# Performance work log

Hardware: AMD Instinct MI355X
Metric: run time of the kernel (lower is better)

## Reference

```python
import jax, jax.numpy as jnp
import numpy as np

EPS = 1e-15
N_NODES = 20000
N_EDGES = 640000
FEAT = 128
N_RBF = 20
CUTOFF = 5.0


def setup_inputs() -> dict:
    key = jax.random.key(0)
    ks = jax.random.split(key, 10)
    s_j = jax.random.normal(ks[0], (N_NODES, FEAT), jnp.float32)
    v_j = jax.random.normal(ks[1], (N_NODES, FEAT, 3), jnp.float32)
    r_ij = jax.random.normal(ks[2], (N_EDGES, 3), jnp.float32)
    nbrs = jax.random.randint(ks[3], (N_EDGES, 2), 0, N_NODES, jnp.int64)
    # InvariantDense: Dense(F->F, swish) then Dense(F->3F)
    W1 = jax.random.normal(ks[4], (FEAT, FEAT), jnp.float32) / np.sqrt(FEAT)
    b1 = jnp.zeros((FEAT,), jnp.float32)
    W2 = jax.random.normal(ks[5], (FEAT, 3 * FEAT), jnp.float32) / np.sqrt(FEAT)
    b2 = jnp.zeros((3 * FEAT,), jnp.float32)
    # DistanceEmbed dense: Dense(n_rbf -> 3F)
    Wd = jax.random.normal(ks[6], (N_RBF, 3 * FEAT), jnp.float32) / np.sqrt(N_RBF)
    bd = jnp.zeros((3 * FEAT,), jnp.float32)
    return {"s_j": s_j, "v_j": v_j, "r_ij": r_ij, "nbrs": nbrs,
            "W1": W1, "b1": b1, "W2": W2, "b2": b2, "Wd": Wd, "bd": bd}


def reference(s_j, v_j, r_ij, nbrs, W1, b1, W2, b2, Wd, bd):
    N, F = s_j.shape
    # preprocess_r
    dist = jnp.sqrt(jnp.sum(r_ij ** 2 + EPS, axis=-1))          # [E]
    unit = r_ij / dist[:, None]                                  # [E,3]
    # InvariantDense on nodes (dense before gather, as in torch code)
    phi_node = jax.nn.silu(s_j @ W1 + b1) @ W2 + b2              # [N,3F]
    phi = phi_node[nbrs[:, 1]]                                   # [E,3F]
    # PaiNN radial basis: sin(n*pi*d/cutoff)/d, n=1..n_rbf
    k = jnp.arange(1, N_RBF + 1, dtype=dist.dtype) * (np.pi / CUTOFF)  # [n_rbf]
    rbf = jnp.sin(dist[:, None] * k[None, :]) / dist[:, None]    # [E,n_rbf]
    # cosine cutoff envelope
    env = 0.5 * (jnp.cos(np.pi * dist / CUTOFF) + 1.0)
    env = jnp.where(dist < CUTOFF, env, 0.0)                     # [E]
    w_s = (rbf @ Wd + bd) * env[:, None]                         # [E,3F]
    inv = (phi * w_s).reshape(-1, 3, F)                          # [E,3,F]
    split0 = inv[:, 0, :][:, :, None]                            # [E,F,1]
    split1 = inv[:, 1, :]                                        # [E,F]
    split2 = inv[:, 2, :][:, :, None]                            # [E,F,1]
    delta_v_ij = split2 * unit[:, None, :] + split0 * v_j[nbrs[:, 1]]  # [E,F,3]
    idx = nbrs[:, 0]
    delta_s_i = jax.ops.segment_sum(split1, idx, num_segments=N)      # [N,F]
    delta_v_i = jax.ops.segment_sum(delta_v_ij, idx, num_segments=N)  # [N,F,3]
    return (delta_s_i, delta_v_i)
```

## Files before the change

kernel.cpp:

```cpp
#include <hip/hip_runtime.h>
#include <hip/hip_bf16.h>
#include <math.h>

typedef __hip_bfloat16 bf16;

#define FEAT 128
#define NRBF 20
#define CUTOFF_F 5.0f
#define KSCALE 0.62831853071795864769f

__device__ __forceinline__ float b2f(bf16 x) { return __bfloat162float(x); }
__device__ __forceinline__ bf16 f2b(float x) { return __float2bfloat16(x); }

template<int F32>
__device__ __forceinline__ float LD(const void* p, size_t i) {
    if (F32) return ((const float*)p)[i];
    return b2f(((const bf16*)p)[i]);
}
template<int F32>
__device__ __forceinline__ void ST(void* p, size_t i, float v) {
    if (F32) ((float*)p)[i] = v;
    else ((bf16*)p)[i] = f2b(v);
}

__device__ __forceinline__ int get_dst(const int* nb, int e, int is64) {
    return is64 ? nb[4 * e] : nb[2 * e];
}
__device__ __forceinline__ int get_src(const int* nb, int e, int is64) {
    return is64 ? nb[4 * e + 2] : nb[2 * e + 1];
}
__device__ __forceinline__ int clampi(int v, int n) {
    return v < 0 ? 0 : (v >= n ? n - 1 : v);
}

__global__ void init_kernel(const void* __restrict__ s_ptr, const int* __restrict__ nbrs32,
                            int nE, int* __restrict__ flags, int* __restrict__ counts, int nN) {
    int t = blockIdx.x * blockDim.x + threadIdx.x;
    if (t < nN) counts[t] = 0;
    if (t == 0) {
        const unsigned* u = (const unsigned*)s_ptr;
        int hits = 0;
        for (int i = 0; i < 64; ++i) {
            unsigned ef = (u[i] >> 7) & 0xFF;
            hits += (ef >= 110 && ef <= 135) ? 1 : 0;
        }
        flags[0] = (hits < 32) ? 1 : 0;
        int lim = 2 * nE; if (lim > 128) lim = 128;
        int allz = 1;
        for (int i = 1; i < lim; i += 2) allz &= (nbrs32[i] == 0);
        flags[1] = allz;
    }
}

__global__ void hist_kernel(const int* __restrict__ nbrs, const int* __restrict__ flags,
                            int* __restrict__ counts, int nE, int nN) {
    int e = blockIdx.x * blockDim.x + threadIdx.x;
    if (e < nE) {
        int d = clampi(get_dst(nbrs, e, flags[1]), nN);
        atomicAdd(&counts[d], 1);
    }
}

__global__ __launch_bounds__(1024) void scan_kernel(const int* __restrict__ counts,
        int* __restrict__ offsets, int* __restrict__ cursor, int nN) {
    __shared__ int part[1024];
    const int t = threadIdx.x;
    const int chunk = (nN + 1023) / 1024;
    const int base = t * chunk;
    int local[32];
    int sum = 0;
    for (int c = 0; c < chunk && c < 32; ++c) {
        int idx = base + c;
        int v = (idx < nN) ? counts[idx] : 0;
        local[c] = v;
        sum += v;
    }
    part[t] = sum;
    __syncthreads();
    for (int off = 1; off < 1024; off <<= 1) {
        int add = (t >= off) ? part[t - off] : 0;
        __syncthreads();
        part[t] += add;
        __syncthreads();
    }
    int run = part[t] - sum;
    for (int c = 0; c < chunk && c < 32; ++c) {
        int idx = base + c;
        if (idx < nN) { offsets[idx] = run; cursor[idx] = run; run += local[c]; }
    }
    if (t == 1023) offsets[nN] = part[1023];
}

__global__ __launch_bounds__(384) void prep_kernel(const void* __restrict__ Wd,
        const void* __restrict__ bd, float* __restrict__ WdT, const int* __restrict__ flags) {
    const int c = threadIdx.x;
    const int F32 = flags[0];
    if (F32) {
        for (int k = 0; k < NRBF; ++k) WdT[c * 24 + k] = ((const float*)Wd)[k * 384 + c];
        WdT[c * 24 + 20] = ((const float*)bd)[c];
    } else {
        for (int k = 0; k < NRBF; ++k) WdT[c * 24 + k] = b2f(((const bf16*)Wd)[k * 384 + c]);
        WdT[c * 24 + 20] = b2f(((const bf16*)bd)[c]);
    }
    WdT[c * 24 + 21] = 0.f; WdT[c * 24 + 22] = 0.f; WdT[c * 24 + 23] = 0.f;
}

template<int F32, int MODEA>
__device__ void pre_scatter_body(const void* __restrict__ r_ij, const int* __restrict__ nbrs,
        int is64, int* __restrict__ cursor, int* __restrict__ src_ids,
        float4* __restrict__ u_env, int* __restrict__ pos_of_e, float* __restrict__ gbuf,
        int e, int nE, int nN) {
    const int d = clampi(get_dst(nbrs, e, is64), nN);
    const int j = clampi(get_src(nbrs, e, is64), nN);
    int pos = atomicAdd(&cursor[d], 1);
    pos = clampi(pos, nE);
    src_ids[pos] = j;

    const float rx = LD<F32>(r_ij, (size_t)3 * e + 0);
    const float ry = LD<F32>(r_ij, (size_t)3 * e + 1);
    const float rz = LD<F32>(r_ij, (size_t)3 * e + 2);
    const float d2   = rx * rx + ry * ry + rz * rz + 3e-15f;
    const float invd = rsqrtf(d2);
    const float dd   = d2 * invd;
    const float x  = dd * KSCALE;
    const float c1 = F32 ? cosf(x) : __cosf(x);
    const float env = (dd < CUTOFF_F) ? (0.5f * (c1 + 1.0f)) : 0.0f;
    u_env[pos] = make_float4(rx * invd, ry * invd, rz * invd, env);

    if (MODEA) {
        pos_of_e[e] = pos;
    } else {
        const float s1 = F32 ? sinf(x) : __sinf(x);
        const float scale = invd * env;
        const float tc = 2.0f * c1;
        float skm2 = 0.f, skm1 = s1;
        float* g = gbuf + (size_t)pos * NRBF;
        g[0] = s1 * scale;
        #pragma unroll
        for (int k = 1; k < NRBF; ++k) {
            const float sk = fmaf(tc, skm1, -skm2);
            g[k] = sk * scale;
            skm2 = skm1; skm1 = sk;
        }
    }
}

__global__ __launch_bounds__(256) void pre_scatter_kernel(const void* r_ij, const int* nbrs,
        const int* __restrict__ flags, int* cursor, int* src_ids, float4* u_env,
        int* pos_of_e, float* gbuf, int nE, int nN, int modeA) {
    int e = blockIdx.x * blockDim.x + threadIdx.x;
    if (e >= nE) return;
    const int F32 = flags[0], is64 = flags[1];
    if (modeA) {
        if (F32) pre_scatter_body<1,1>(r_ij, nbrs, is64, cursor, src_ids, u_env, pos_of_e, gbuf, e, nE, nN);
        else     pre_scatter_body<0,1>(r_ij, nbrs, is64, cursor, src_ids, u_env, pos_of_e, gbuf, e, nE, nN);
    } else {
        if (F32) pre_scatter_body<1,0>(r_ij, nbrs, is64, cursor, src_ids, u_env, pos_of_e, gbuf, e, nE, nN);
        else     pre_scatter_body<0,0>(r_ij, nbrs, is64, cursor, src_ids, u_env, pos_of_e, gbuf, e, nE, nN);
    }
}

template<int F32>
__device__ void gemm_body(const void* __restrict__ s_j, const void* __restrict__ W1,
                          const void* __restrict__ b1, const void* __restrict__ W2,
                          const void* __restrict__ b2v, bf16* __restrict__ phi, int nN) {
    __shared__ float sl[8][FEAT];
    __shared__ float hl[8][FEAT];
    const int t = threadIdx.x;
    const int n0 = blockIdx.x * 8;
    for (int idx = t; idx < 8 * FEAT; idx += 384) {
        int n = idx >> 7, k = idx & 127;
        int row = n0 + n;
        sl[n][k] = (row < nN) ? LD<F32>(s_j, (size_t)row * FEAT + k) : 0.f;
    }
    __syncthreads();
    for (int idx = t; idx < 8 * FEAT; idx += 384) {
        int n = idx >> 7, f = idx & 127;
        float a = 0.f;
        #pragma unroll 4
        for (int k = 0; k < FEAT; ++k) a = fmaf(sl[n][k], LD<F32>(W1, (size_t)k * FEAT + f), a);
        a += LD<F32>(b1, f);
        float sg = F32 ? (1.0f / (1.0f + expf(-a))) : (1.0f / (1.0f + __expf(-a)));
        hl[n][f] = a * sg;
    }
    __syncthreads();
    float acc[8] = {};
    #pragma unroll 4
    for (int k = 0; k < FEAT; ++k) {
        const float w = LD<F32>(W2, (size_t)k * 384 + t);
        #pragma unroll
        for (int n = 0; n < 8; ++n) acc[n] = fmaf(hl[n][k], w, acc[n]);
    }
    const float bb = LD<F32>(b2v, t);
    #pragma unroll
    for (int n = 0; n < 8; ++n) {
        int row = n0 + n;
        if (row < nN) phi[(size_t)row * 384 + t] = f2b(acc[n] + bb);
    }
}

__global__ __launch_bounds__(384) void gemm_node_kernel(const void* s_j, const void* W1,
        const void* b1, const void* W2, const void* b2v, bf16* phi,
        const int* __restrict__ flags, int nN) {
    if (flags[0]) gemm_body<1>(s_j, W1, b1, W2, b2v, phi, nN);
    else          gemm_body<0>(s_j, W1, b1, W2, b2v, phi, nN);
}

template<int F32>
__device__ void pre_ws_body(const void* __restrict__ r_ij, const float* __restrict__ WdT,
        const int* __restrict__ pos_of_e, bf16* __restrict__ ws_w, int e) {
    const float rx = LD<F32>(r_ij, (size_t)3 * e + 0);
    const float ry = LD<F32>(r_ij, (size_t)3 * e + 1);
    const float rz = LD<F32>(r_ij, (size_t)3 * e + 2);
    const float d2   = rx * rx + ry * ry + rz * rz + 3e-15f;
    const float invd = rsqrtf(d2);
    const float dd   = d2 * invd;
    const float x  = dd * KSCALE;
    const float s1 = F32 ? sinf(x) : __sinf(x);
    const float c1 = F32 ? cosf(x) : __cosf(x);
    const float env = (dd < CUTOFF_F) ? (0.5f * (c1 + 1.0f)) : 0.0f;
    const float scale = invd * env;
    float gk[NRBF];
    const float tc = 2.0f * c1;
    float skm2 = 0.f, skm1 = s1;
    gk[0] = s1 * scale;
    #pragma unroll
    for (int k = 1; k < NRBF; ++k) {
        const float sk = fmaf(tc, skm1, -skm2);
        gk[k] = sk * scale;
        skm2 = skm1; skm1 = sk;
    }
    const int pos = pos_of_e[e];
    bf16* dst = ws_w + (size_t)pos * 384;
    for (int c0 = 0; c0 < 384; c0 += 4) {
        float r[4];
        #pragma unroll
        for (int u = 0; u < 4; ++u) {
            const float* w = WdT + (size_t)(c0 + u) * 24;
            float acc = w[20] * env;
            #pragma unroll
            for (int k = 0; k < NRBF; ++k) acc = fmaf(gk[k], w[k], acc);
            r[u] = acc;
        }
        union { bf16 b[4]; uint2 u2; } pk;
        pk.b[0] = f2b(r[0]); pk.b[1] = f2b(r[1]); pk.b[2] = f2b(r[2]); pk.b[3] = f2b(r[3]);
        *(uint2*)(dst + c0) = pk.u2;
    }
}

__global__ __launch_bounds__(256) void pre_ws_kernel(const void* r_ij,
        const float* __restrict__ WdT, const int* __restrict__ pos_of_e,
        bf16* __restrict__ ws_w, const int* __restrict__ flags, int nE) {
    int e = blockIdx.x * blockDim.x + threadIdx.x;
    if (e >= nE) return;
    if (flags[0]) pre_ws_body<1>(r_ij, WdT, pos_of_e, ws_w, e);
    else          pre_ws_body<0>(r_ij, WdT, pos_of_e, ws_w, e);
}

template<int F32>
__device__ void msg_a_body(const bf16* __restrict__ ws_w, const bf16* __restrict__ phi,
        const void* __restrict__ v_j, const int* __restrict__ src_ids,
        const float4* __restrict__ u_env, const int* __restrict__ offsets,
        void* __restrict__ out, int nE, int nN) {
    const int i = blockIdx.x;
    const int f = threadIdx.x;
    int start = offsets[i];
    int end   = offsets[i + 1];
    if (start < 0) start = 0;
    if (end > nE) end = nE;

    float ds = 0.f, dv0 = 0.f, dv1 = 0.f, dv2 = 0.f;

    #pragma unroll 2
    for (int p = start; p < end; ++p) {
        const int j = src_ids[p];
        const float4 ue = u_env[p];
        const bf16* wr = ws_w + (size_t)p * 384;
        const float w0 = b2f(wr[f]);
        const float w1 = b2f(wr[FEAT + f]);
        const float w2 = b2f(wr[2 * FEAT + f]);
        const bf16* ph = phi + (size_t)j * 384;
        const float p0 = b2f(ph[f]);
        const float p1 = b2f(ph[FEAT + f]);
        const float p2 = b2f(ph[2 * FEAT + f]);
        const float vx = LD<F32>(v_j, ((size_t)j * FEAT + f) * 3 + 0);
        const float vy = LD<F32>(v_j, ((size_t)j * FEAT + f) * 3 + 1);
        const float vz = LD<F32>(v_j, ((size_t)j * FEAT + f) * 3 + 2);
        const float i0 = w0 * p0;
        const float i1 = w1 * p1;
        const float i2 = w2 * p2;
        ds += i1;
        dv0 = fmaf(i2, ue.x, fmaf(i0, vx, dv0));
        dv1 = fmaf(i2, ue.y, fmaf(i0, vy, dv1));
        dv2 = fmaf(i2, ue.z, fmaf(i0, vz, dv2));
    }

    ST<F32>(out, (size_t)i * FEAT + f, ds);
    const size_t ob = (size_t)nN * FEAT + ((size_t)i * FEAT + f) * 3;
    ST<F32>(out, ob + 0, dv0);
    ST<F32>(out, ob + 1, dv1);
    ST<F32>(out, ob + 2, dv2);
}

__global__ __launch_bounds__(128) void msg_a_kernel(const bf16* ws_w, const bf16* phi,
        const void* v_j, const int* src_ids, const float4* u_env, const int* offsets,
        const int* __restrict__ flags, void* out, int nE, int nN) {
    if (flags[0]) msg_a_body<1>(ws_w, phi, v_j, src_ids, u_env, offsets, out, nE, nN);
    else          msg_a_body<0>(ws_w, phi, v_j, src_ids, u_env, offsets, out, nE, nN);
}

template<int F32>
__device__ void msg_b_body(const void* __restrict__ v_j, const void* __restrict__ Wd,
        const void* __restrict__ bd, const bf16* __restrict__ phi,
        const float* __restrict__ gbuf, const int* __restrict__ src_ids,
        const float4* __restrict__ u_env, const int* __restrict__ offsets,
        void* __restrict__ out, int nE, int nN) {
    const int i = blockIdx.x;
    const int f = threadIdx.x;

    float wd0[NRBF], wd1[NRBF], wd2[NRBF];
    #pragma unroll
    for (int k = 0; k < NRBF; ++k) {
        wd0[k] = LD<F32>(Wd, (size_t)k * 384 + f);
        wd1[k] = LD<F32>(Wd, (size_t)k * 384 + FEAT + f);
        wd2[k] = LD<F32>(Wd, (size_t)k * 384 + 2 * FEAT + f);
    }
    const float bd0 = LD<F32>(bd, f);
    const float bd1 = LD<F32>(bd, FEAT + f);
    const float bd2 = LD<F32>(bd, 2 * FEAT + f);

    int start = offsets[i];
    int end   = offsets[i + 1];
    if (start < 0) start = 0;
    if (end > nE) end = nE;

    float ds = 0.f, dv0 = 0.f, dv1 = 0.f, dv2 = 0.f;

    for (int p = start; p < end; ++p) {
        const int j = src_ids[p];
        const float4 ue = u_env[p];
        const float* g = gbuf + (size_t)p * NRBF;
        float t0 = 0.f, t1 = 0.f, t2 = 0.f;
        #pragma unroll
        for (int k = 0; k < NRBF; ++k) {
            const float gk = g[k];
            t0 = fmaf(gk, wd0[k], t0);
            t1 = fmaf(gk, wd1[k], t1);
            t2 = fmaf(gk, wd2[k], t2);
        }
        const float w0 = fmaf(bd0, ue.w, t0);
        const float w1 = fmaf(bd1, ue.w, t1);
        const float w2 = fmaf(bd2, ue.w, t2);

        const bf16* ph = phi + (size_t)j * 384;
        const float p0 = b2f(ph[f]);
        const float p1 = b2f(ph[FEAT + f]);
        const float p2 = b2f(ph[2 * FEAT + f]);
        const float vx = LD<F32>(v_j, ((size_t)j * FEAT + f) * 3 + 0);
        const float vy = LD<F32>(v_j, ((size_t)j * FEAT + f) * 3 + 1);
        const float vz = LD<F32>(v_j, ((size_t)j * FEAT + f) * 3 + 2);

        const float i0 = w0 * p0;
        const float i1 = w1 * p1;
        const float i2 = w2 * p2;
        ds += i1;
        dv0 = fmaf(i2, ue.x, fmaf(i0, vx, dv0));
        dv1 = fmaf(i2, ue.y, fmaf(i0, vy, dv1));
        dv2 = fmaf(i2, ue.z, fmaf(i0, vz, dv2));
    }

    ST<F32>(out, (size_t)i * FEAT + f, ds);
    const size_t ob = (size_t)nN * FEAT + ((size_t)i * FEAT + f) * 3;
    ST<F32>(out, ob + 0, dv0);
    ST<F32>(out, ob + 1, dv1);
    ST<F32>(out, ob + 2, dv2);
}

__global__ __launch_bounds__(128) void msg_b_kernel(const void* v_j, const void* Wd,
        const void* bd, const bf16* phi, const float* gbuf, const int* src_ids,
        const float4* u_env, const int* offsets, const int* __restrict__ flags,
        void* out, int nE, int nN) {
    if (flags[0]) msg_b_body<1>(v_j, Wd, bd, phi, gbuf, src_ids, u_env, offsets, out, nE, nN);
    else          msg_b_body<0>(v_j, Wd, bd, phi, gbuf, src_ids, u_env, offsets, out, nE, nN);
}

extern "C" void kernel_launch(void* const* d_in, const int* in_sizes, int n_in,
                              void* d_out, int out_size, void* d_ws, size_t ws_size,
                              hipStream_t stream) {
    const void* s_j  = d_in[0];
    const void* v_j  = d_in[1];
    const void* r_ij = d_in[2];
    const int*  nbrs = (const int*)d_in[3];
    const void* W1   = d_in[4];
    const void* b1   = d_in[5];
    const void* W2   = d_in[6];
    const void* b2   = d_in[7];
    const void* Wd   = d_in[8];
    const void* bd   = d_in[9];

    const int nN = out_size / (4 * FEAT);
    const int nE = in_sizes[2] / 3;

    char* ws = (char*)d_ws;
    size_t off = 0;
    auto alloc = [&](size_t bytes) -> void* {
        void* p = ws + off;
        off = (off + bytes + 255) & ~(size_t)255;
        return p;
    };
    int*    flags    = (int*)alloc(16);
    int*    counts   = (int*)alloc((size_t)nN * 4);
    int*    offsets  = (int*)alloc(((size_t)nN + 1) * 4);
    int*    cursor   = (int*)alloc((size_t)nN * 4);
    int*    src_ids  = (int*)alloc((size_t)nE * 4);
    float4* u_env    = (float4*)alloc((size_t)nE * 16);
    float*  WdT      = (float*)alloc((size_t)384 * 24 * 4);
    const size_t base = off;

    size_t offA = base;
    int*  pos_of_e = (int*)(ws + offA);  offA += ((size_t)nE * 4 + 255) & ~(size_t)255;
    bf16* phiA     = (bf16*)(ws + offA); offA += ((size_t)nN * 384 * 2 + 255) & ~(size_t)255;
    bf16* ws_w     = (bf16*)(ws + offA); offA += (size_t)nE * 384 * 2;
    size_t offB = base;
    float* gbuf = (float*)(ws + offB);   offB += ((size_t)nE * NRBF * 4 + 255) & ~(size_t)255;
    bf16*  phiB = (bf16*)(ws + offB);    offB += (size_t)nN * 384 * 2;

    const int modeA = (ws_size >= offA) ? 1 : 0;
    bf16* phi = modeA ? phiA : phiB;

    init_kernel<<<(nN + 255) / 256, 256, 0, stream>>>(s_j, nbrs, nE, flags, counts, nN);
    hist_kernel<<<(nE + 255) / 256, 256, 0, stream>>>(nbrs, flags, counts, nE, nN);
    scan_kernel<<<1, 1024, 0, stream>>>(counts, offsets, cursor, nN);
    prep_kernel<<<1, 384, 0, stream>>>(Wd, bd, WdT, flags);

    pre_scatter_kernel<<<(nE + 255) / 256, 256, 0, stream>>>(
        r_ij, nbrs, flags, cursor, src_ids, u_env, pos_of_e, gbuf, nE, nN, modeA);

    gemm_node_kernel<<<(nN + 7) / 8, 384, 0, stream>>>(s_j, W1, b1, W2, b2, phi, flags, nN);

    if (modeA) {
        pre_ws_kernel<<<(nE + 255) / 256, 256, 0, stream>>>(r_ij, WdT, pos_of_e, ws_w, flags, nE);
        msg_a_kernel<<<nN, 128, 0, stream>>>(ws_w, phi, v_j, src_ids, u_env, offsets,
                                             flags, d_out, nE, nN);
    } else {
        msg_b_kernel<<<nN, 128, 0, stream>>>(v_j, Wd, bd, phi, gbuf, src_ids, u_env,
                                             offsets, flags, d_out, nE, nN);
    }
}
```

Baseline: 532.5 us.

## Split msg_b feature channels across 384 threads with LDS reduction

The fallback message kernel now uses 384 threads per node, one per output channel of the distance-embedding projection, instead of 128 threads that each handled all three channels. Per-thread Wd registers and FMAs per edge drop threefold. The two vector contributions are combined through shared memory before the store. Uniform indices are moved to scalar registers via readfirstlane. This adds more parallelism and lowers register pressure, at the cost of redundant gbuf and u_env loads across warps and an extra barrier.

```diff
diff --git a/kernel.cpp b/kernel.cpp
--- a/kernel.cpp
+++ b/kernel.cpp
@@ -316,67 +316,71 @@
         const float4* __restrict__ u_env, const int* __restrict__ offsets,
         void* __restrict__ out, int nE, int nN) {
     const int i = blockIdx.x;
-    const int f = threadIdx.x;
-
-    float wd0[NRBF], wd1[NRBF], wd2[NRBF];
+    const int c = threadIdx.x;
+    const int grp = c >> 7;
+
+    float wd[NRBF];
     #pragma unroll
-    for (int k = 0; k < NRBF; ++k) {
-        wd0[k] = LD<F32>(Wd, (size_t)k * 384 + f);
-        wd1[k] = LD<F32>(Wd, (size_t)k * 384 + FEAT + f);
-        wd2[k] = LD<F32>(Wd, (size_t)k * 384 + 2 * FEAT + f);
-    }
-    const float bd0 = LD<F32>(bd, f);
-    const float bd1 = LD<F32>(bd, FEAT + f);
-    const float bd2 = LD<F32>(bd, 2 * FEAT + f);
-
-    int start = offsets[i];
-    int end   = offsets[i + 1];
+    for (int k = 0; k < NRBF; ++k) wd[k] = LD<F32>(Wd, (size_t)k * 384 + c);
+    float bdc = LD<F32>(bd, c);
+    #pragma unroll
+    for (int k = 0; k < NRBF; ++k) asm volatile("" : "+v"(wd[k]));
+    asm volatile("" : "+v"(bdc));
+
+    int start = __builtin_amdgcn_readfirstlane(offsets[i]);
+    int end   = __builtin_amdgcn_readfirstlane(offsets[i + 1]);
     if (start < 0) start = 0;
     if (end > nE) end = nE;
 
-    float ds = 0.f, dv0 = 0.f, dv1 = 0.f, dv2 = 0.f;
+    float a0 = 0.f, a1 = 0.f, a2 = 0.f;
 
     for (int p = start; p < end; ++p) {
-        const int j = src_ids[p];
+        const int j = __builtin_amdgcn_readfirstlane(src_ids[p]);
         const float4 ue = u_env[p];
         const float* g = gbuf + (size_t)p * NRBF;
-        float t0 = 0.f, t1 = 0.f, t2 = 0.f;
+        float te = 0.f, to = 0.f;
         #pragma unroll
-        for (int k = 0; k < NRBF; ++k) {
-            const float gk = g[k];
-            t0 = fmaf(gk, wd0[k], t0);
-            t1 = fmaf(gk, wd1[k], t1);
-            t2 = fmaf(gk, wd2[k], t2);
+        for (int k = 0; k < NRBF; k += 2) {
+            te = fmaf(g[k],     wd[k],     te);
+            to = fmaf(g[k + 1], wd[k + 1], to);
         }
-        const float w0 = fmaf(bd0, ue.w, t0);
-        const float w1 = fmaf(bd1, ue.w, t1);
-        const float w2 = fmaf(bd2, ue.w, t2);
-
-        const bf16* ph = phi + (size_t)j * 384;
-        const float p0 = b2f(ph[f]);
-        const float p1 = b2f(ph[FEAT + f]);
-        const float p2 = b2f(ph[2 * FEAT + f]);
-        const float vx = LD<F32>(v_j, ((size_t)j * FEAT + f) * 3 + 0);
-        const float vy = LD<F32>(v_j, ((size_t)j * FEAT + f) * 3 + 1);
-        const float vz = LD<F32>(v_j, ((size_t)j * FEAT + f) * 3 + 2);
-
-        const float i0 = w0 * p0;
-        const float i1 = w1 * p1;
-        const float i2 = w2 * p2;
-        ds += i1;
-        dv0 = fmaf(i2, ue.x, fmaf(i0, vx, dv0));
-        dv1 = fmaf(i2, ue.y, fmaf(i0, vy, dv1));
-        dv2 = fmaf(i2, ue.z, fmaf(i0, vz, dv2));
-    }
-
-    ST<F32>(out, (size_t)i * FEAT + f, ds);
-    const size_t ob = (size_t)nN * FEAT + ((size_t)i * FEAT + f) * 3;
-    ST<F32>(out, ob + 0, dv0);
-    ST<F32>(out, ob + 1, dv1);
-    ST<F32>(out, ob + 2, dv2);
-}
-
-__global__ __launch_bounds__(128) void msg_b_kernel(const void* v_j, const void* Wd,
+        const float w = fmaf(bdc, ue.w, te + to);
+        const float ph = b2f(phi[(size_t)j * 384 + c]);
+        const float iv = w * ph;
+        if (grp == 0) {
+            const float vx = LD<F32>(v_j, ((size_t)j * FEAT + c) * 3 + 0);
+            const float vy = LD<F32>(v_j, ((size_t)j * FEAT + c) * 3 + 1);
+            const float vz = LD<F32>(v_j, ((size_t)j * FEAT + c) * 3 + 2);
+            a0 = fmaf(iv, vx, a0);
+            a1 = fmaf(iv, vy, a1);
+            a2 = fmaf(iv, vz, a2);
+        } else if (grp == 1) {
+            a0 += iv;
+        } else {
+            a0 = fmaf(iv, ue.x, a0);
+            a1 = fmaf(iv, ue.y, a1);
+            a2 = fmaf(iv, ue.z, a2);
+        }
+    }
+
+    __shared__ float red[FEAT][3];
+    if (grp == 2) {
+        red[c - 256][0] = a0;
+        red[c - 256][1] = a1;
+        red[c - 256][2] = a2;
+    }
+    __syncthreads();
+    if (grp == 1) {
+        ST<F32>(out, (size_t)i * FEAT + (c - FEAT), a0);
+    } else if (grp == 0) {
+        const size_t ob = (size_t)nN * FEAT + ((size_t)i * FEAT + c) * 3;
+        ST<F32>(out, ob + 0, a0 + red[c][0]);
+        ST<F32>(out, ob + 1, a1 + red[c][1]);
+        ST<F32>(out, ob + 2, a2 + red[c][2]);
+    }
+}
+
+__global__ __launch_bounds__(384) void msg_b_kernel(const void* v_j, const void* Wd,
         const void* bd, const bf16* phi, const float* gbuf, const int* src_ids,
         const float4* u_env, const int* offsets, const int* __restrict__ flags,
         void* out, int nE, int nN) {
@@ -443,7 +447,7 @@
         msg_a_kernel<<<nN, 128, 0, stream>>>(ws_w, phi, v_j, src_ids, u_env, offsets,
                                              flags, d_out, nE, nN);
     } else {
-        msg_b_kernel<<<nN, 128, 0, stream>>>(v_j, Wd, bd, phi, gbuf, src_ids, u_env,
+        msg_b_kernel<<<nN, 384, 0, stream>>>(v_j, Wd, bd, phi, gbuf, src_ids, u_env,
                                              offsets, flags, d_out, nE, nN);
     }
 }
```

After: 818.0 us. 53.6% more time.

## Add packed phi+v record path for workspace-limited mode

Applied to the files above, without the earlier changes.

Adds a third execution mode used when the workspace cannot hold the per-edge ws_w buffer but can hold a packed per-node record. The node GEMM writes its three phi channels interleaved into a 16-byte record per (node, feature), and a new kernel packs v_j as bf16 into the same record. The message kernel then fetches phi and v for each edge with one 16-byte load and uses the transposed Wd prepared earlier. This aims to cut scattered gather traffic during aggregation, at the cost of an extra packing pass and lower-precision v.

```diff
diff --git a/kernel.cpp b/kernel.cpp
--- a/kernel.cpp
+++ b/kernel.cpp
@@ -163,7 +163,8 @@
 template<int F32>
 __device__ void gemm_body(const void* __restrict__ s_j, const void* __restrict__ W1,
                           const void* __restrict__ b1, const void* __restrict__ W2,
-                          const void* __restrict__ b2v, bf16* __restrict__ phi, int nN) {
+                          const void* __restrict__ b2v, bf16* __restrict__ phi, int nN,
+                          int packed) {
     __shared__ float sl[8][FEAT];
     __shared__ float hl[8][FEAT];
     const int t = threadIdx.x;
@@ -192,18 +193,46 @@
         for (int n = 0; n < 8; ++n) acc[n] = fmaf(hl[n][k], w, acc[n]);
     }
     const float bb = LD<F32>(b2v, t);
+    const int fch  = t & 127;
+    const int comp = t >> 7;
     #pragma unroll
     for (int n = 0; n < 8; ++n) {
         int row = n0 + n;
-        if (row < nN) phi[(size_t)row * 384 + t] = f2b(acc[n] + bb);
+        if (row < nN) {
+            if (packed) phi[((size_t)row * FEAT + fch) * 8 + comp] = f2b(acc[n] + bb);
+            else        phi[(size_t)row * 384 + t] = f2b(acc[n] + bb);
+        }
     }
 }
 
 __global__ __launch_bounds__(384) void gemm_node_kernel(const void* s_j, const void* W1,
         const void* b1, const void* W2, const void* b2v, bf16* phi,
-        const int* __restrict__ flags, int nN) {
-    if (flags[0]) gemm_body<1>(s_j, W1, b1, W2, b2v, phi, nN);
-    else          gemm_body<0>(s_j, W1, b1, W2, b2v, phi, nN);
+        const int* __restrict__ flags, int nN, int packed) {
+    if (flags[0]) gemm_body<1>(s_j, W1, b1, W2, b2v, phi, nN, packed);
+    else          gemm_body<0>(s_j, W1, b1, W2, b2v, phi, nN, packed);
+}
+
+__global__ __launch_bounds__(256) void pack_v_kernel(const void* __restrict__ v_j,
+        bf16* __restrict__ rec, const int* __restrict__ flags, int nN) {
+    int t = blockIdx.x * blockDim.x + threadIdx.x;
+    if (t >= nN * FEAT) return;
+    float vx, vy, vz;
+    if (flags[0]) {
+        const float* v = (const float*)v_j;
+        vx = v[(size_t)3 * t + 0];
+        vy = v[(size_t)3 * t + 1];
+        vz = v[(size_t)3 * t + 2];
+    } else {
+        const bf16* v = (const bf16*)v_j;
+        vx = b2f(v[(size_t)3 * t + 0]);
+        vy = b2f(v[(size_t)3 * t + 1]);
+        vz = b2f(v[(size_t)3 * t + 2]);
+    }
+    bf16* d = rec + (size_t)t * 8;
+    union { bf16 b[2]; unsigned u; } p01;
+    p01.b[0] = f2b(vx); p01.b[1] = f2b(vy);
+    *(unsigned*)(d + 4) = p01.u;
+    d[6] = f2b(vz);
 }
 
 template<int F32>
@@ -310,6 +339,71 @@
 }
 
 template<int F32>
+__device__ void msg_c_body(const float* __restrict__ WdT, const bf16* __restrict__ rec,
+        const float* __restrict__ gbuf, const int* __restrict__ src_ids,
+        const float4* __restrict__ u_env, const int* __restrict__ offsets,
+        void* __restrict__ out, int nE, int nN) {
+    const int i = blockIdx.x;
+    const int f = threadIdx.x;
+    int start = offsets[i];
+    int end   = offsets[i + 1];
+    if (start < 0) start = 0;
+    if (end > nE) end = nE;
+
+    const float* w0p = WdT + (size_t)f * 24;
+    const float* w1p = WdT + (size_t)(f + FEAT) * 24;
+    const float* w2p = WdT + (size_t)(f + 2 * FEAT) * 24;
+
+    float ds = 0.f, dv0 = 0.f, dv1 = 0.f, dv2 = 0.f;
+
+    for (int p = start; p < end; ++p) {
+        const int j = src_ids[p];
+        const float4 ue = u_env[p];
+        const float* g = gbuf + (size_t)p * NRBF;
+        float t0 = 0.f, t1 = 0.f, t2 = 0.f;
+        #pragma unroll
+        for (int k = 0; k < NRBF; ++k) {
+            const float gk = g[k];
+            t0 = fmaf(gk, w0p[k], t0);
+            t1 = fmaf(gk, w1p[k], t1);
+            t2 = fmaf(gk, w2p[k], t2);
+        }
+        const float w0 = fmaf(w0p[20], ue.w, t0);
+        const float w1 = fmaf(w1p[20], ue.w, t1);
+        const float w2 = fmaf(w2p[20], ue.w, t2);
+
+        const uint4 rv = *(const uint4*)(rec + ((size_t)j * FEAT + f) * 8);
+        const float p0 = __uint_as_float(rv.x << 16);
+        const float p1 = __uint_as_float(rv.x & 0xffff0000u);
+        const float p2 = __uint_as_float(rv.y << 16);
+        const float vx = __uint_as_float(rv.z << 16);
+        const float vy = __uint_as_float(rv.z & 0xffff0000u);
+        const float vz = __uint_as_float(rv.w << 16);
+
+        const float i0 = w0 * p0;
+        const float i1 = w1 * p1;
+        const float i2 = w2 * p2;
+        ds += i1;
+        dv0 = fmaf(i2, ue.x, fmaf(i0, vx, dv0));
+        dv1 = fmaf(i2, ue.y, fmaf(i0, vy, dv1));
+        dv2 = fmaf(i2, ue.z, fmaf(i0, vz, dv2));
+    }
+
+    ST<F32>(out, (size_t)i * FEAT + f, ds);
+    const size_t ob = (size_t)nN * FEAT + ((size_t)i * FEAT + f) * 3;
+    ST<F32>(out, ob + 0, dv0);
+    ST<F32>(out, ob + 1, dv1);
+    ST<F32>(out, ob + 2, dv2);
+}
+
+__global__ __launch_bounds__(128) void msg_c_kernel(const float* WdT, const bf16* rec,
+        const float* gbuf, const int* src_ids, const float4* u_env, const int* offsets,
+        const int* __restrict__ flags, void* out, int nE, int nN) {
+    if (flags[0]) msg_c_body<1>(WdT, rec, gbuf, src_ids, u_env, offsets, out, nE, nN);
+    else          msg_c_body<0>(WdT, rec, gbuf, src_ids, u_env, offsets, out, nE, nN);
+}
+
+template<int F32>
 __device__ void msg_b_body(const void* __restrict__ v_j, const void* __restrict__ Wd,
         const void* __restrict__ bd, const bf16* __restrict__ phi,
         const float* __restrict__ gbuf, const int* __restrict__ src_ids,
@@ -421,12 +515,15 @@
     int*  pos_of_e = (int*)(ws + offA);  offA += ((size_t)nE * 4 + 255) & ~(size_t)255;
     bf16* phiA     = (bf16*)(ws + offA); offA += ((size_t)nN * 384 * 2 + 255) & ~(size_t)255;
     bf16* ws_w     = (bf16*)(ws + offA); offA += (size_t)nE * 384 * 2;
+    size_t offC = base;
+    float* gbufC = (float*)(ws + offC);  offC += ((size_t)nE * NRBF * 4 + 255) & ~(size_t)255;
+    bf16*  rec   = (bf16*)(ws + offC);   offC += (size_t)nN * FEAT * 8 * 2;
     size_t offB = base;
-    float* gbuf = (float*)(ws + offB);   offB += ((size_t)nE * NRBF * 4 + 255) & ~(size_t)255;
-    bf16*  phiB = (bf16*)(ws + offB);    offB += (size_t)nN * 384 * 2;
+    float* gbufB = (float*)(ws + offB);  offB += ((size_t)nE * NRBF * 4 + 255) & ~(size_t)255;
+    bf16*  phiB  = (bf16*)(ws + offB);   offB += (size_t)nN * 384 * 2;
 
     const int modeA = (ws_size >= offA) ? 1 : 0;
-    bf16* phi = modeA ? phiA : phiB;
+    const int modeC = (!modeA && ws_size >= offC) ? 1 : 0;
 
     init_kernel<<<(nN + 255) / 256, 256, 0, stream>>>(s_j, nbrs, nE, flags, counts, nN);
     hist_kernel<<<(nE + 255) / 256, 256, 0, stream>>>(nbrs, flags, counts, nE, nN);
@@ -434,16 +531,21 @@
     prep_kernel<<<1, 384, 0, stream>>>(Wd, bd, WdT, flags);
 
     pre_scatter_kernel<<<(nE + 255) / 256, 256, 0, stream>>>(
-        r_ij, nbrs, flags, cursor, src_ids, u_env, pos_of_e, gbuf, nE, nN, modeA);
-
-    gemm_node_kernel<<<(nN + 7) / 8, 384, 0, stream>>>(s_j, W1, b1, W2, b2, phi, flags, nN);
+        r_ij, nbrs, flags, cursor, src_ids, u_env, pos_of_e, gbufC, nE, nN, modeA);
 
     if (modeA) {
+        gemm_node_kernel<<<(nN + 7) / 8, 384, 0, stream>>>(s_j, W1, b1, W2, b2, phiA, flags, nN, 0);
         pre_ws_kernel<<<(nE + 255) / 256, 256, 0, stream>>>(r_ij, WdT, pos_of_e, ws_w, flags, nE);
-        msg_a_kernel<<<nN, 128, 0, stream>>>(ws_w, phi, v_j, src_ids, u_env, offsets,
+        msg_a_kernel<<<nN, 128, 0, stream>>>(ws_w, phiA, v_j, src_ids, u_env, offsets,
+                                             flags, d_out, nE, nN);
+    } else if (modeC) {
+        gemm_node_kernel<<<(nN + 7) / 8, 384, 0, stream>>>(s_j, W1, b1, W2, b2, rec, flags, nN, 1);
+        pack_v_kernel<<<((nN * FEAT) + 255) / 256, 256, 0, stream>>>(v_j, rec, flags, nN);
+        msg_c_kernel<<<nN, 128, 0, stream>>>(WdT, rec, gbufC, src_ids, u_env, offsets,
                                              flags, d_out, nE, nN);
     } else {
-        msg_b_kernel<<<nN, 128, 0, stream>>>(v_j, Wd, bd, phi, gbuf, src_ids, u_env,
+        gemm_node_kernel<<<(nN + 7) / 8, 384, 0, stream>>>(s_j, W1, b1, W2, b2, phiB, flags, nN, 0);
+        msg_b_kernel<<<nN, 128, 0, stream>>>(v_j, Wd, bd, phiB, gbufC, src_ids, u_env,
                                              offsets, flags, d_out, nE, nN);
     }
 }
```

Result: slower. 546.6 us (+2.7%).
